# Kernel tuning notes

Hardware: AMD Instinct MI355X
Metric: run time of the kernel (lower is better)

Reference implementation:

```python
import jax, jax.numpy as jnp
import numpy as np
import math

B, S, D = 16, 4096, 64

def setup_inputs() -> dict:
    key = jax.random.key(0)
    kq, kk, kv = jax.random.split(key, 3)
    query = jax.random.normal(kq, (B, S, D), dtype=jnp.float32)
    k_ = jax.random.normal(kk, (B, S, D), dtype=jnp.float32)
    value = jax.random.normal(kv, (B, S, D), dtype=jnp.float32)
    # causal mask: 1 = allowed, 0 = masked (set to -inf), broadcast over batch
    mask = jnp.tril(jnp.ones((S, S), dtype=jnp.int32))[None, :, :]
    return {"query": query, "key": k_, "value": value, "mask": mask, "key_dim": D}

def reference(query, key, value, mask, key_dim):
    # scores: [B, S, S] = Q @ K^T / sqrt(dk)
    scores = jnp.einsum('bqd,bkd->bqk', query, key) / math.sqrt(key_dim)
    scores = jnp.where(mask == 0, -jnp.inf, scores)
    attn = jax.nn.softmax(scores, axis=-1)
    return jnp.einsum('bqk,bkd->bqd', attn, value)
```

## Files before the change

kernel.cpp:

```cpp
#include <hip/hip_runtime.h>

typedef _Float16 half8 __attribute__((ext_vector_type(8)));
typedef __fp16 fp16x2 __attribute__((ext_vector_type(2)));
typedef float f32x4 __attribute__((ext_vector_type(4)));
typedef unsigned int uint32x2 __attribute__((ext_vector_type(2)));

union Frag { half8 v; unsigned int u32[4]; uint4 u4; };
union Pack4 { _Float16 h[4]; unsigned int u[2]; };
union H2U { fp16x2 h; unsigned int u; };

constexpr int S = 4096;
constexpr int D = 64;
constexpr int NB = 16;
constexpr int LTS = 72;

__device__ __forceinline__ float ex2(float x) {
#if __has_builtin(__builtin_amdgcn_exp2f)
    return __builtin_amdgcn_exp2f(x);
#else
    return exp2f(x);
#endif
}

__global__ __launch_bounds__(256)
void prep_kernel(const float* __restrict__ K, const float* __restrict__ V,
                 _Float16* __restrict__ K16, _Float16* __restrict__ VT) {
    __shared__ float tl[64 * 66];
    const int tid = threadIdx.x;
    const int s0 = blockIdx.x * 64;
    const int b  = blockIdx.y;
    const float* Kb = K + ((size_t)b * S + s0) * D;
    const float* Vb = V + ((size_t)b * S + s0) * D;
    _Float16* K16b = K16 + ((size_t)b * S + s0) * D;

    #pragma unroll
    for (int i = 0; i < 2; ++i) {
        int e8 = tid + 256 * i;
        float4 a = ((const float4*)Kb)[2 * e8];
        float4 c = ((const float4*)Kb)[2 * e8 + 1];
        Frag f;
        f.v[0]=(_Float16)a.x; f.v[1]=(_Float16)a.y; f.v[2]=(_Float16)a.z; f.v[3]=(_Float16)a.w;
        f.v[4]=(_Float16)c.x; f.v[5]=(_Float16)c.y; f.v[6]=(_Float16)c.z; f.v[7]=(_Float16)c.w;
        ((uint4*)K16b)[e8] = f.u4;
    }
    #pragma unroll
    for (int i = 0; i < 4; ++i) {
        int fi = tid + 256 * i;
        int r = fi >> 4, c4 = (fi & 15) << 2;
        float4 v = *(const float4*)(Vb + (size_t)r * D + c4);
        float2* p = (float2*)&tl[r * 66 + c4];
        p[0] = make_float2(v.x, v.y);
        p[1] = make_float2(v.z, v.w);
    }
    __syncthreads();
    _Float16* VTb = VT + (size_t)b * D * S;
    #pragma unroll
    for (int i = 0; i < 2; ++i) {
        int fi = tid + 256 * i;
        int d = fi >> 3, s8 = (fi & 7) << 3;
        Frag f;
        #pragma unroll
        for (int j = 0; j < 8; ++j) f.v[j] = (_Float16)tl[(s8 + j) * 66 + d];
        *(uint4*)(VTb + (size_t)d * S + s0 + s8) = f.u4;
    }
}

template <int SPLIT>
__device__ __forceinline__
void fattn_body(const float* __restrict__ Q, const _Float16* __restrict__ K16,
                const _Float16* __restrict__ VT16, float* __restrict__ Out,
                _Float16* __restrict__ OP, float* __restrict__ LP,
                int b, int J, int t0, int t1, int h) {
    __shared__ __align__(16) _Float16 kt[64 * LTS];
    __shared__ __align__(16) _Float16 vt[64 * LTS];

    const int tid  = threadIdx.x;
    const int lane = tid & 63;
    const int wave = tid >> 6;
    const int ln   = lane & 15;
    const int quad = lane >> 4;

    const float* Qb = Q + (size_t)b * S * D;
    const _Float16* Kb = K16 + (size_t)b * S * D;
    const _Float16* VTb = VT16 + (size_t)b * D * S;

    const float qscale = 0.125f * 1.44269504088896340736f;
    const int qrow_base = J * 128 + wave * 32;
    const int tw = (qrow_base + 31) >> 6;

    Frag qf[2][2];
    #pragma unroll
    for (int qg = 0; qg < 2; ++qg) {
        const float* qrow = Qb + (size_t)(qrow_base + qg * 16 + ln) * D + quad * 8;
        #pragma unroll
        for (int ks = 0; ks < 2; ++ks) {
            float4 a = *(const float4*)(qrow + ks * 32);
            float4 c = *(const float4*)(qrow + ks * 32 + 4);
            Frag f;
            f.v[0]=(_Float16)(a.x*qscale); f.v[1]=(_Float16)(a.y*qscale);
            f.v[2]=(_Float16)(a.z*qscale); f.v[3]=(_Float16)(a.w*qscale);
            f.v[4]=(_Float16)(c.x*qscale); f.v[5]=(_Float16)(c.y*qscale);
            f.v[6]=(_Float16)(c.z*qscale); f.v[7]=(_Float16)(c.w*qscale);
            qf[qg][ks] = f;
        }
    }

    f32x4 o[2][4] = {};
    float l_acc[2] = {0.f, 0.f};

    const int r0_ = tid >> 3,         c8_0 = (tid & 7) << 3;
    const int r1_ = (tid + 256) >> 3, c8_1 = ((tid + 256) & 7) << 3;
    uint4 pk0, pk1, pv0, pv1;
    auto issue = [&](int tt) {
        const int kk0 = tt * 64;
        pk0 = *(const uint4*)(Kb + (size_t)(kk0 + r0_) * D + c8_0);
        pv0 = *(const uint4*)(VTb + (size_t)r0_ * S + kk0 + c8_0);
        pk1 = *(const uint4*)(Kb + (size_t)(kk0 + r1_) * D + c8_1);
        pv1 = *(const uint4*)(VTb + (size_t)r1_ * S + kk0 + c8_1);
    };
    if (t0 < t1) issue(t0);

    for (int t = t0; t < t1; ++t) {
        const int k0 = t * 64;
        __syncthreads();
        *(uint4*)(kt + r0_ * LTS + c8_0) = pk0;
        *(uint4*)(vt + r0_ * LTS + c8_0) = pv0;
        *(uint4*)(kt + r1_ * LTS + c8_1) = pk1;
        *(uint4*)(vt + r1_ * LTS + c8_1) = pv1;
        __syncthreads();
        if (t + 1 < t1) issue(t + 1);

        #pragma unroll
        for (int ks = 0; ks < 2; ++ks) {
            unsigned w[2][2][2];
            #pragma unroll
            for (int cl = 0; cl < 2; ++cl) {
                const int ct = ks * 2 + cl;
                Frag kf0, kf1;
                kf0.u4 = *(const uint4*)(kt + (ct * 16 + ln) * LTS + quad * 8);
                kf1.u4 = *(const uint4*)(kt + (ct * 16 + ln) * LTS + 32 + quad * 8);
                #pragma unroll
                for (int qg = 0; qg < 2; ++qg) {
                    f32x4 acc = {0.f, 0.f, 0.f, 0.f};
                    acc = __builtin_amdgcn_mfma_f32_16x16x32_f16(kf0.v, qf[qg][0].v, acc, 0, 0, 0);
                    acc = __builtin_amdgcn_mfma_f32_16x16x32_f16(kf1.v, qf[qg][1].v, acc, 0, 0, 0);
                    if (t >= tw) {
                        int keyb = k0 + ct * 16 + quad * 4;
                        int qrow = qrow_base + qg * 16 + ln;
                        #pragma unroll
                        for (int r = 0; r < 4; ++r)
                            if (keyb + r > qrow) acc[r] = -1e30f;
                    }
                    float p0 = ex2(acc[0]), p1 = ex2(acc[1]);
                    float p2 = ex2(acc[2]), p3 = ex2(acc[3]);
                    l_acc[qg] += (p0 + p1) + (p2 + p3);
#if __has_builtin(__builtin_amdgcn_cvt_pkrtz)
                    H2U c0, c1;
                    c0.h = __builtin_amdgcn_cvt_pkrtz(p0, p1);
                    c1.h = __builtin_amdgcn_cvt_pkrtz(p2, p3);
                    w[qg][cl][0] = c0.u;
                    w[qg][cl][1] = c1.u;
#else
                    Pack4 pk;
                    pk.h[0] = (_Float16)p0; pk.h[1] = (_Float16)p1;
                    pk.h[2] = (_Float16)p2; pk.h[3] = (_Float16)p3;
                    w[qg][cl][0] = pk.u[0];
                    w[qg][cl][1] = pk.u[1];
#endif
                }
            }

            Frag pf[2];
            #pragma unroll
            for (int qg = 0; qg < 2; ++qg) {
                unsigned x0 = w[qg][0][0], y0 = w[qg][1][0];
                unsigned x1 = w[qg][0][1], y1 = w[qg][1][1];
#if __has_builtin(__builtin_amdgcn_permlane32_swap) && __has_builtin(__builtin_amdgcn_permlane16_swap)
                uint32x2 r;
                r = __builtin_amdgcn_permlane32_swap(x0, y0, false, false); x0 = r[0]; y0 = r[1];
                r = __builtin_amdgcn_permlane32_swap(x1, y1, false, false); x1 = r[0]; y1 = r[1];
                r = __builtin_amdgcn_permlane16_swap(x0, y0, false, false); x0 = r[0]; y0 = r[1];
                r = __builtin_amdgcn_permlane16_swap(x1, y1, false, false); x1 = r[0]; y1 = r[1];
#else
                asm volatile("s_nop 1\n\tv_permlane32_swap_b32 %0, %1\n\ts_nop 1"
                             : "+v"(x0), "+v"(y0));
                asm volatile("v_permlane32_swap_b32 %0, %1\n\ts_nop 1"
                             : "+v"(x1), "+v"(y1));
                asm volatile("v_permlane16_swap_b32 %0, %1\n\ts_nop 1"
                             : "+v"(x0), "+v"(y0));
                asm volatile("v_permlane16_swap_b32 %0, %1\n\ts_nop 1"
                             : "+v"(x1), "+v"(y1));
#endif
                pf[qg].u32[0] = x0; pf[qg].u32[1] = x1;
                pf[qg].u32[2] = y0; pf[qg].u32[3] = y1;
            }

            #pragma unroll
            for (int sub = 0; sub < 4; ++sub) {
                Frag vf;
                vf.u4 = *(const uint4*)(vt + (sub * 16 + ln) * LTS + ks * 32 + quad * 8);
                #pragma unroll
                for (int qg = 0; qg < 2; ++qg)
                    o[qg][sub] = __builtin_amdgcn_mfma_f32_16x16x32_f16(pf[qg].v, vf.v, o[qg][sub], 0, 0, 0);
            }
        }
    }

    float lf[2];
    #pragma unroll
    for (int qg = 0; qg < 2; ++qg) {
        float x = l_acc[qg];
        x += __shfl_xor(x, 16, 64);
        x += __shfl_xor(x, 32, 64);
        lf[qg] = x;
    }

    if (SPLIT) {
        _Float16* OPb = OP + (size_t)(((b * 32 + J) * 4 + h)) * 8192;
        float* LPb = LP + (size_t)(((b * 32 + J) * 4 + h)) * 128;
        #pragma unroll
        for (int qg = 0; qg < 2; ++qg) {
            if (quad == 0) LPb[wave * 32 + qg * 16 + ln] = lf[qg];
            #pragma unroll
            for (int r = 0; r < 4; ++r) {
                float lrow = __shfl(lf[qg], quad * 4 + r, 64);
                float inv = (lrow > 0.f) ? (1.0f / lrow) : 0.f;
                #pragma unroll
                for (int sub = 0; sub < 4; ++sub)
                    OPb[(wave * 32 + qg * 16 + quad * 4 + r) * 64 + sub * 16 + ln] =
                        (_Float16)(o[qg][sub][r] * inv);
            }
        }
    } else {
        float* Ob = Out + (size_t)b * S * D;
        #pragma unroll
        for (int qg = 0; qg < 2; ++qg) {
            #pragma unroll
            for (int r = 0; r < 4; ++r) {
                float lrow = __shfl(lf[qg], quad * 4 + r, 64);
                float inv = 1.0f / lrow;
                #pragma unroll
                for (int sub = 0; sub < 4; ++sub)
                    Ob[(size_t)(qrow_base + qg * 16 + quad * 4 + r) * D + sub * 16 + ln] =
                        o[qg][sub][r] * inv;
            }
        }
    }
}

__global__ __launch_bounds__(256, 4)
void fattn_split_kernel(const float* __restrict__ Q, const _Float16* __restrict__ K16,
                        const _Float16* __restrict__ VT16,
                        _Float16* __restrict__ OP, float* __restrict__ LP) {
    const int bx = blockIdx.x;
    const int J = 31 - (bx >> 6);
    const int h = (bx >> 4) & 3;
    const int b = bx & 15;
    const int n  = 2 * J + 2;
    const int t0 = (h * n) >> 2;
    const int t1 = ((h + 1) * n) >> 2;
    fattn_body<1>(Q, K16, VT16, nullptr, OP, LP, b, J, t0, t1, h);
}

__global__ __launch_bounds__(256, 4)
void fattn_kernel(const float* __restrict__ Q, const _Float16* __restrict__ K16,
                  const _Float16* __restrict__ VT16, float* __restrict__ Out) {
    const int bx = blockIdx.x;
    const int J = 31 - (bx >> 4);
    const int b = bx & 15;
    fattn_body<0>(Q, K16, VT16, Out, nullptr, nullptr, b, J, 0, 2 * J + 2, 0);
}

__global__ __launch_bounds__(256)
void reduce_kernel(const _Float16* __restrict__ OP, const float* __restrict__ LP,
                   float* __restrict__ Out) {
    const int rb = blockIdx.x;
    const int b  = rb & 15;
    const int J  = rb >> 4;
    const int tid = threadIdx.x;
    const _Float16* p = OP + (size_t)(b * 32 + J) * 4 * 8192;
    const float* l = LP + (size_t)(b * 32 + J) * 4 * 128;
    float* Ob = Out + (size_t)b * S * D + (size_t)J * 8192;
    #pragma unroll
    for (int i = 0; i < 4; ++i) {
        int e8 = tid + 256 * i;
        int q  = e8 >> 3;
        float lw[4], lsum = 0.f;
        #pragma unroll
        for (int hh = 0; hh < 4; ++hh) { lw[hh] = l[hh * 128 + q]; lsum += lw[hh]; }
        float inv = 1.0f / lsum;
        float acc[8] = {};
        #pragma unroll
        for (int hh = 0; hh < 4; ++hh) {
            half8 v = *(const half8*)(p + (size_t)hh * 8192 + e8 * 8);
            #pragma unroll
            for (int j = 0; j < 8; ++j) acc[j] += lw[hh] * (float)v[j];
        }
        float4 r0, r1;
        r0.x = acc[0]*inv; r0.y = acc[1]*inv; r0.z = acc[2]*inv; r0.w = acc[3]*inv;
        r1.x = acc[4]*inv; r1.y = acc[5]*inv; r1.z = acc[6]*inv; r1.w = acc[7]*inv;
        ((float4*)Ob)[2 * e8]     = r0;
        ((float4*)Ob)[2 * e8 + 1] = r1;
    }
}

extern "C" void kernel_launch(void* const* d_in, const int* in_sizes, int n_in,
                              void* d_out, int out_size, void* d_ws, size_t ws_size,
                              hipStream_t stream) {
    const float* Q = (const float*)d_in[0];
    const float* K = (const float*)d_in[1];
    const float* V = (const float*)d_in[2];
    float* O = (float*)d_out;

    const size_t prepBytes = (size_t)NB * S * D * 2;
    _Float16* K16  = (_Float16*)d_ws;
    _Float16* VT16 = (_Float16*)((char*)d_ws + prepBytes);

    const size_t opOff = 2 * prepBytes;
    const size_t opBytes = (size_t)NB * 32 * 4 * 8192 * 2;
    const size_t lpOff = opOff + opBytes;
    const size_t lpBytes = (size_t)NB * 32 * 4 * 128 * 4;
    const size_t need = lpOff + lpBytes;

    hipLaunchKernelGGL(prep_kernel, dim3(S / 64, NB), dim3(256), 0, stream, K, V, K16, VT16);

    if (ws_size >= need) {
        _Float16* OP = (_Float16*)((char*)d_ws + opOff);
        float* LP = (float*)((char*)d_ws + lpOff);
        hipLaunchKernelGGL(fattn_split_kernel, dim3(128 * NB), dim3(256), 0, stream,
                           Q, K16, VT16, OP, LP);
        hipLaunchKernelGGL(reduce_kernel, dim3(32 * NB), dim3(256), 0, stream, OP, LP, O);
    } else {
        hipLaunchKernelGGL(fattn_kernel, dim3(32 * NB), dim3(256), 0, stream, Q, K16, VT16, O);
    }
}
```

Measured before the change: 186.6 us.

## Fuse split-K reduction into attention kernel via last-block atomic counter

Removes the separate reduce kernel launch. Each split block increments a per-(batch, query-tile) atomic counter after writing its partial output, and the fourth block to finish performs the weighted combine and writes the final output. Counters are zeroed in the prep kernel. This saves a launch and lets the reduction overlap other tiles' work, at the cost of fences, an atomic per block, and extra register and LDS pressure in the main kernel.

```diff
diff --git a/kernel.cpp b/kernel.cpp
--- a/kernel.cpp
+++ b/kernel.cpp
@@ -24,11 +24,13 @@
 
 __global__ __launch_bounds__(256)
 void prep_kernel(const float* __restrict__ K, const float* __restrict__ V,
-                 _Float16* __restrict__ K16, _Float16* __restrict__ VT) {
+                 _Float16* __restrict__ K16, _Float16* __restrict__ VT,
+                 int* __restrict__ CNT) {
     __shared__ float tl[64 * 66];
     const int tid = threadIdx.x;
     const int s0 = blockIdx.x * 64;
     const int b  = blockIdx.y;
+    if (b == 0 && blockIdx.x < 2) CNT[blockIdx.x * 256 + tid] = 0;
     const float* Kb = K + ((size_t)b * S + s0) * D;
     const float* Vb = V + ((size_t)b * S + s0) * D;
     _Float16* K16b = K16 + ((size_t)b * S + s0) * D;
@@ -70,9 +72,11 @@
 void fattn_body(const float* __restrict__ Q, const _Float16* __restrict__ K16,
                 const _Float16* __restrict__ VT16, float* __restrict__ Out,
                 _Float16* __restrict__ OP, float* __restrict__ LP,
+                int* __restrict__ CNT,
                 int b, int J, int t0, int t1, int h) {
     __shared__ __align__(16) _Float16 kt[64 * LTS];
     __shared__ __align__(16) _Float16 vt[64 * LTS];
+    __shared__ int last_flag;
 
     const int tid  = threadIdx.x;
     const int lane = tid & 63;
@@ -231,6 +235,42 @@
                         (_Float16)(o[qg][sub][r] * inv);
             }
         }
+
+        __threadfence();
+        __syncthreads();
+        if (tid == 0) {
+            int old = __hip_atomic_fetch_add(&CNT[b * 32 + J], 1,
+                                             __ATOMIC_ACQ_REL, __HIP_MEMORY_SCOPE_AGENT);
+            last_flag = (old == 3);
+        }
+        __syncthreads();
+        if (!last_flag) return;
+        __threadfence();
+
+        const _Float16* p = OP + (size_t)(b * 32 + J) * 4 * 8192;
+        const float* l = LP + (size_t)(b * 32 + J) * 4 * 128;
+        float* Ob = Out + (size_t)b * S * D + (size_t)J * 8192;
+        #pragma unroll
+        for (int i = 0; i < 4; ++i) {
+            int e8 = tid + 256 * i;
+            int q  = e8 >> 3;
+            float lw[4], lsum = 0.f;
+            #pragma unroll
+            for (int hh = 0; hh < 4; ++hh) { lw[hh] = l[hh * 128 + q]; lsum += lw[hh]; }
+            float inv = 1.0f / lsum;
+            float acc[8] = {};
+            #pragma unroll
+            for (int hh = 0; hh < 4; ++hh) {
+                half8 v = *(const half8*)(p + (size_t)hh * 8192 + e8 * 8);
+                #pragma unroll
+                for (int j = 0; j < 8; ++j) acc[j] += lw[hh] * (float)v[j];
+            }
+            float4 r0, r1;
+            r0.x = acc[0]*inv; r0.y = acc[1]*inv; r0.z = acc[2]*inv; r0.w = acc[3]*inv;
+            r1.x = acc[4]*inv; r1.y = acc[5]*inv; r1.z = acc[6]*inv; r1.w = acc[7]*inv;
+            ((float4*)Ob)[2 * e8]     = r0;
+            ((float4*)Ob)[2 * e8 + 1] = r1;
+        }
     } else {
         float* Ob = Out + (size_t)b * S * D;
         #pragma unroll
@@ -251,7 +291,8 @@
 __global__ __launch_bounds__(256, 4)
 void fattn_split_kernel(const float* __restrict__ Q, const _Float16* __restrict__ K16,
                         const _Float16* __restrict__ VT16,
-                        _Float16* __restrict__ OP, float* __restrict__ LP) {
+                        _Float16* __restrict__ OP, float* __restrict__ LP,
+                        int* __restrict__ CNT, float* __restrict__ Out) {
     const int bx = blockIdx.x;
     const int J = 31 - (bx >> 6);
     const int h = (bx >> 4) & 3;
@@ -259,7 +300,7 @@
     const int n  = 2 * J + 2;
     const int t0 = (h * n) >> 2;
     const int t1 = ((h + 1) * n) >> 2;
-    fattn_body<1>(Q, K16, VT16, nullptr, OP, LP, b, J, t0, t1, h);
+    fattn_body<1>(Q, K16, VT16, Out, OP, LP, CNT, b, J, t0, t1, h);
 }
 
 __global__ __launch_bounds__(256, 4)
@@ -268,40 +309,7 @@
     const int bx = blockIdx.x;
     const int J = 31 - (bx >> 4);
     const int b = bx & 15;
-    fattn_body<0>(Q, K16, VT16, Out, nullptr, nullptr, b, J, 0, 2 * J + 2, 0);
-}
-
-__global__ __launch_bounds__(256)
-void reduce_kernel(const _Float16* __restrict__ OP, const float* __restrict__ LP,
-                   float* __restrict__ Out) {
-    const int rb = blockIdx.x;
-    const int b  = rb & 15;
-    const int J  = rb >> 4;
-    const int tid = threadIdx.x;
-    const _Float16* p = OP + (size_t)(b * 32 + J) * 4 * 8192;
-    const float* l = LP + (size_t)(b * 32 + J) * 4 * 128;
-    float* Ob = Out + (size_t)b * S * D + (size_t)J * 8192;
-    #pragma unroll
-    for (int i = 0; i < 4; ++i) {
-        int e8 = tid + 256 * i;
-        int q  = e8 >> 3;
-        float lw[4], lsum = 0.f;
-        #pragma unroll
-        for (int hh = 0; hh < 4; ++hh) { lw[hh] = l[hh * 128 + q]; lsum += lw[hh]; }
-        float inv = 1.0f / lsum;
-        float acc[8] = {};
-        #pragma unroll
-        for (int hh = 0; hh < 4; ++hh) {
-            half8 v = *(const half8*)(p + (size_t)hh * 8192 + e8 * 8);
-            #pragma unroll
-            for (int j = 0; j < 8; ++j) acc[j] += lw[hh] * (float)v[j];
-        }
-        float4 r0, r1;
-        r0.x = acc[0]*inv; r0.y = acc[1]*inv; r0.z = acc[2]*inv; r0.w = acc[3]*inv;
-        r1.x = acc[4]*inv; r1.y = acc[5]*inv; r1.z = acc[6]*inv; r1.w = acc[7]*inv;
-        ((float4*)Ob)[2 * e8]     = r0;
-        ((float4*)Ob)[2 * e8 + 1] = r1;
-    }
+    fattn_body<0>(Q, K16, VT16, Out, nullptr, nullptr, nullptr, b, J, 0, 2 * J + 2, 0);
 }
 
 extern "C" void kernel_launch(void* const* d_in, const int* in_sizes, int n_in,
@@ -320,16 +328,18 @@
     const size_t opBytes = (size_t)NB * 32 * 4 * 8192 * 2;
     const size_t lpOff = opOff + opBytes;
     const size_t lpBytes = (size_t)NB * 32 * 4 * 128 * 4;
-    const size_t need = lpOff + lpBytes;
-
-    hipLaunchKernelGGL(prep_kernel, dim3(S / 64, NB), dim3(256), 0, stream, K, V, K16, VT16);
+    const size_t cntOff = lpOff + lpBytes;
+    const size_t cntBytes = 512 * sizeof(int);
+    const size_t need = cntOff + cntBytes;
+
+    int* CNT = (int*)((char*)d_ws + cntOff);
+    hipLaunchKernelGGL(prep_kernel, dim3(S / 64, NB), dim3(256), 0, stream, K, V, K16, VT16, CNT);
 
     if (ws_size >= need) {
         _Float16* OP = (_Float16*)((char*)d_ws + opOff);
         float* LP = (float*)((char*)d_ws + lpOff);
         hipLaunchKernelGGL(fattn_split_kernel, dim3(128 * NB), dim3(256), 0, stream,
-                           Q, K16, VT16, OP, LP);
-        hipLaunchKernelGGL(reduce_kernel, dim3(32 * NB), dim3(256), 0, stream, OP, LP, O);
+                           Q, K16, VT16, OP, LP, CNT, O);
     } else {
         hipLaunchKernelGGL(fattn_kernel, dim3(32 * NB), dim3(256), 0, stream, Q, K16, VT16, O);
     }
```

Result: slower. 611.6 us (+227.8%).

## Fuse K/V fp16 conversion and V transpose into attention kernel, drop prep pass

Applied to the files above, without the earlier changes.

Removes the separate prep kernel that converted K to fp16 and wrote a transposed fp16 V to workspace. The attention kernel now loads fp32 K and V tiles directly, converts them in registers, and transposes V through an extra shared-memory staging buffer, with V prefetched two tiles ahead. This saves one kernel launch and the workspace write and read-back, but doubles the global bytes loaded per tile (fp32 instead of fp16) across the many redundant causal tile reads. It also adds conversion work, more LDS traffic and an extra shared buffer that may hurt occupancy.

```diff
diff --git a/kernel.cpp b/kernel.cpp
--- a/kernel.cpp
+++ b/kernel.cpp
@@ -6,7 +6,6 @@
 typedef unsigned int uint32x2 __attribute__((ext_vector_type(2)));
 
 union Frag { half8 v; unsigned int u32[4]; uint4 u4; };
-union Pack4 { _Float16 h[4]; unsigned int u[2]; };
 union H2U { fp16x2 h; unsigned int u; };
 
 constexpr int S = 4096;
@@ -22,57 +21,38 @@
 #endif
 }
 
-__global__ __launch_bounds__(256)
-void prep_kernel(const float* __restrict__ K, const float* __restrict__ V,
-                 _Float16* __restrict__ K16, _Float16* __restrict__ VT) {
-    __shared__ float tl[64 * 66];
-    const int tid = threadIdx.x;
-    const int s0 = blockIdx.x * 64;
-    const int b  = blockIdx.y;
-    const float* Kb = K + ((size_t)b * S + s0) * D;
-    const float* Vb = V + ((size_t)b * S + s0) * D;
-    _Float16* K16b = K16 + ((size_t)b * S + s0) * D;
-
-    #pragma unroll
-    for (int i = 0; i < 2; ++i) {
-        int e8 = tid + 256 * i;
-        float4 a = ((const float4*)Kb)[2 * e8];
-        float4 c = ((const float4*)Kb)[2 * e8 + 1];
-        Frag f;
-        f.v[0]=(_Float16)a.x; f.v[1]=(_Float16)a.y; f.v[2]=(_Float16)a.z; f.v[3]=(_Float16)a.w;
-        f.v[4]=(_Float16)c.x; f.v[5]=(_Float16)c.y; f.v[6]=(_Float16)c.z; f.v[7]=(_Float16)c.w;
-        ((uint4*)K16b)[e8] = f.u4;
-    }
-    #pragma unroll
-    for (int i = 0; i < 4; ++i) {
-        int fi = tid + 256 * i;
-        int r = fi >> 4, c4 = (fi & 15) << 2;
-        float4 v = *(const float4*)(Vb + (size_t)r * D + c4);
-        float2* p = (float2*)&tl[r * 66 + c4];
-        p[0] = make_float2(v.x, v.y);
-        p[1] = make_float2(v.z, v.w);
-    }
-    __syncthreads();
-    _Float16* VTb = VT + (size_t)b * D * S;
-    #pragma unroll
-    for (int i = 0; i < 2; ++i) {
-        int fi = tid + 256 * i;
-        int d = fi >> 3, s8 = (fi & 7) << 3;
-        Frag f;
-        #pragma unroll
-        for (int j = 0; j < 8; ++j) f.v[j] = (_Float16)tl[(s8 + j) * 66 + d];
-        *(uint4*)(VTb + (size_t)d * S + s0 + s8) = f.u4;
-    }
+__device__ __forceinline__ void cvt16(const float4* a, uint4& lo, uint4& hi) {
+#if __has_builtin(__builtin_amdgcn_cvt_pkrtz)
+    H2U h0,h1,h2,h3,h4,h5,h6,h7;
+    h0.h = __builtin_amdgcn_cvt_pkrtz(a[0].x, a[0].y);
+    h1.h = __builtin_amdgcn_cvt_pkrtz(a[0].z, a[0].w);
+    h2.h = __builtin_amdgcn_cvt_pkrtz(a[1].x, a[1].y);
+    h3.h = __builtin_amdgcn_cvt_pkrtz(a[1].z, a[1].w);
+    h4.h = __builtin_amdgcn_cvt_pkrtz(a[2].x, a[2].y);
+    h5.h = __builtin_amdgcn_cvt_pkrtz(a[2].z, a[2].w);
+    h6.h = __builtin_amdgcn_cvt_pkrtz(a[3].x, a[3].y);
+    h7.h = __builtin_amdgcn_cvt_pkrtz(a[3].z, a[3].w);
+    lo = make_uint4(h0.u, h1.u, h2.u, h3.u);
+    hi = make_uint4(h4.u, h5.u, h6.u, h7.u);
+#else
+    Frag f, g;
+    f.v[0]=(_Float16)a[0].x; f.v[1]=(_Float16)a[0].y; f.v[2]=(_Float16)a[0].z; f.v[3]=(_Float16)a[0].w;
+    f.v[4]=(_Float16)a[1].x; f.v[5]=(_Float16)a[1].y; f.v[6]=(_Float16)a[1].z; f.v[7]=(_Float16)a[1].w;
+    g.v[0]=(_Float16)a[2].x; g.v[1]=(_Float16)a[2].y; g.v[2]=(_Float16)a[2].z; g.v[3]=(_Float16)a[2].w;
+    g.v[4]=(_Float16)a[3].x; g.v[5]=(_Float16)a[3].y; g.v[6]=(_Float16)a[3].z; g.v[7]=(_Float16)a[3].w;
+    lo = f.u4; hi = g.u4;
+#endif
 }
 
 template <int SPLIT>
 __device__ __forceinline__
-void fattn_body(const float* __restrict__ Q, const _Float16* __restrict__ K16,
-                const _Float16* __restrict__ VT16, float* __restrict__ Out,
+void fattn_body(const float* __restrict__ Q, const float* __restrict__ K,
+                const float* __restrict__ V, float* __restrict__ Out,
                 _Float16* __restrict__ OP, float* __restrict__ LP,
                 int b, int J, int t0, int t1, int h) {
     __shared__ __align__(16) _Float16 kt[64 * LTS];
     __shared__ __align__(16) _Float16 vt[64 * LTS];
+    __shared__ __align__(16) _Float16 vs[64 * LTS];
 
     const int tid  = threadIdx.x;
     const int lane = tid & 63;
@@ -81,8 +61,8 @@
     const int quad = lane >> 4;
 
     const float* Qb = Q + (size_t)b * S * D;
-    const _Float16* Kb = K16 + (size_t)b * S * D;
-    const _Float16* VTb = VT16 + (size_t)b * D * S;
+    const float* Kb = K + (size_t)b * S * D;
+    const float* Vb = V + (size_t)b * S * D;
 
     const float qscale = 0.125f * 1.44269504088896340736f;
     const int qrow_base = J * 128 + wave * 32;
@@ -108,27 +88,59 @@
     f32x4 o[2][4] = {};
     float l_acc[2] = {0.f, 0.f};
 
-    const int r0_ = tid >> 3,         c8_0 = (tid & 7) << 3;
-    const int r1_ = (tid + 256) >> 3, c8_1 = ((tid + 256) & 7) << 3;
-    uint4 pk0, pk1, pv0, pv1;
-    auto issue = [&](int tt) {
-        const int kk0 = tt * 64;
-        pk0 = *(const uint4*)(Kb + (size_t)(kk0 + r0_) * D + c8_0);
-        pv0 = *(const uint4*)(VTb + (size_t)r0_ * S + kk0 + c8_0);
-        pk1 = *(const uint4*)(Kb + (size_t)(kk0 + r1_) * D + c8_1);
-        pv1 = *(const uint4*)(VTb + (size_t)r1_ * S + kk0 + c8_1);
+    const int sr = tid >> 2;
+    const int sq = (tid & 3) << 4;
+    const int td2 = tid >> 3;
+    const int ts8 = (tid & 7) << 3;
+
+    float4 kA[4], vA[4];
+    auto loadK = [&](int tt) {
+        const float4* p = (const float4*)(Kb + (size_t)(tt * 64 + sr) * D + sq);
+        kA[0] = p[0]; kA[1] = p[1]; kA[2] = p[2]; kA[3] = p[3];
     };
-    if (t0 < t1) issue(t0);
+    auto loadV = [&](int tt) {
+        const float4* p = (const float4*)(Vb + (size_t)(tt * 64 + sr) * D + sq);
+        vA[0] = p[0]; vA[1] = p[1]; vA[2] = p[2]; vA[3] = p[3];
+    };
+
+    if (t0 < t1) {
+        loadV(t0); loadK(t0);
+        uint4 lo, hi; cvt16(vA, lo, hi);
+        *(uint4*)(vs + sr * LTS + sq)     = lo;
+        *(uint4*)(vs + sr * LTS + sq + 8) = hi;
+        loadV(t0 + 1 < t1 ? t0 + 1 : t0);
+    }
 
     for (int t = t0; t < t1; ++t) {
         const int k0 = t * 64;
         __syncthreads();
-        *(uint4*)(kt + r0_ * LTS + c8_0) = pk0;
-        *(uint4*)(vt + r0_ * LTS + c8_0) = pv0;
-        *(uint4*)(kt + r1_ * LTS + c8_1) = pk1;
-        *(uint4*)(vt + r1_ * LTS + c8_1) = pv1;
+
+        {
+            uint4 lo, hi; cvt16(kA, lo, hi);
+            *(uint4*)(kt + sr * LTS + sq)     = lo;
+            *(uint4*)(kt + sr * LTS + sq + 8) = hi;
+        }
+        {
+            const unsigned* col = (const unsigned*)vs + ts8 * (LTS / 2) + td2;
+            unsigned x0 = col[0],   x1 = col[36],  x2 = col[72],  x3 = col[108];
+            unsigned x4 = col[144], x5 = col[180], x6 = col[216], x7 = col[252];
+            uint4 rlo, rhi;
+            rlo.x = (x0 & 0xffffu) | (x1 << 16);  rlo.y = (x2 & 0xffffu) | (x3 << 16);
+            rlo.z = (x4 & 0xffffu) | (x5 << 16);  rlo.w = (x6 & 0xffffu) | (x7 << 16);
+            rhi.x = (x0 >> 16) | (x1 & 0xffff0000u);  rhi.y = (x2 >> 16) | (x3 & 0xffff0000u);
+            rhi.z = (x4 >> 16) | (x5 & 0xffff0000u);  rhi.w = (x6 >> 16) | (x7 & 0xffff0000u);
+            *(uint4*)(vt + (2 * td2) * LTS + ts8)     = rlo;
+            *(uint4*)(vt + (2 * td2 + 1) * LTS + ts8) = rhi;
+        }
         __syncthreads();
-        if (t + 1 < t1) issue(t + 1);
+
+        if (t + 1 < t1) {
+            uint4 lo, hi; cvt16(vA, lo, hi);
+            *(uint4*)(vs + sr * LTS + sq)     = lo;
+            *(uint4*)(vs + sr * LTS + sq + 8) = hi;
+            loadK(t + 1);
+            loadV(t + 2 < t1 ? t + 2 : t + 1);
+        }
 
         #pragma unroll
         for (int ks = 0; ks < 2; ++ks) {
@@ -161,11 +173,11 @@
                     w[qg][cl][0] = c0.u;
                     w[qg][cl][1] = c1.u;
 #else
-                    Pack4 pk;
-                    pk.h[0] = (_Float16)p0; pk.h[1] = (_Float16)p1;
-                    pk.h[2] = (_Float16)p2; pk.h[3] = (_Float16)p3;
-                    w[qg][cl][0] = pk.u[0];
-                    w[qg][cl][1] = pk.u[1];
+                    Frag pk;
+                    pk.v[0] = (_Float16)p0; pk.v[1] = (_Float16)p1;
+                    pk.v[2] = (_Float16)p2; pk.v[3] = (_Float16)p3;
+                    w[qg][cl][0] = pk.u32[0];
+                    w[qg][cl][1] = pk.u32[1];
 #endif
                 }
             }
@@ -249,8 +261,8 @@
 }
 
 __global__ __launch_bounds__(256, 4)
-void fattn_split_kernel(const float* __restrict__ Q, const _Float16* __restrict__ K16,
-                        const _Float16* __restrict__ VT16,
+void fattn_split_kernel(const float* __restrict__ Q, const float* __restrict__ K,
+                        const float* __restrict__ V,
                         _Float16* __restrict__ OP, float* __restrict__ LP) {
     const int bx = blockIdx.x;
     const int J = 31 - (bx >> 6);
@@ -259,16 +271,16 @@
     const int n  = 2 * J + 2;
     const int t0 = (h * n) >> 2;
     const int t1 = ((h + 1) * n) >> 2;
-    fattn_body<1>(Q, K16, VT16, nullptr, OP, LP, b, J, t0, t1, h);
+    fattn_body<1>(Q, K, V, nullptr, OP, LP, b, J, t0, t1, h);
 }
 
 __global__ __launch_bounds__(256, 4)
-void fattn_kernel(const float* __restrict__ Q, const _Float16* __restrict__ K16,
-                  const _Float16* __restrict__ VT16, float* __restrict__ Out) {
+void fattn_kernel(const float* __restrict__ Q, const float* __restrict__ K,
+                  const float* __restrict__ V, float* __restrict__ Out) {
     const int bx = blockIdx.x;
     const int J = 31 - (bx >> 4);
     const int b = bx & 15;
-    fattn_body<0>(Q, K16, VT16, Out, nullptr, nullptr, b, J, 0, 2 * J + 2, 0);
+    fattn_body<0>(Q, K, V, Out, nullptr, nullptr, b, J, 0, 2 * J + 2, 0);
 }
 
 __global__ __launch_bounds__(256)
@@ -312,25 +324,17 @@
     const float* V = (const float*)d_in[2];
     float* O = (float*)d_out;
 
-    const size_t prepBytes = (size_t)NB * S * D * 2;
-    _Float16* K16  = (_Float16*)d_ws;
-    _Float16* VT16 = (_Float16*)((char*)d_ws + prepBytes);
-
-    const size_t opOff = 2 * prepBytes;
     const size_t opBytes = (size_t)NB * 32 * 4 * 8192 * 2;
-    const size_t lpOff = opOff + opBytes;
     const size_t lpBytes = (size_t)NB * 32 * 4 * 128 * 4;
-    const size_t need = lpOff + lpBytes;
-
-    hipLaunchKernelGGL(prep_kernel, dim3(S / 64, NB), dim3(256), 0, stream, K, V, K16, VT16);
+    const size_t need = opBytes + lpBytes;
 
     if (ws_size >= need) {
-        _Float16* OP = (_Float16*)((char*)d_ws + opOff);
-        float* LP = (float*)((char*)d_ws + lpOff);
+        _Float16* OP = (_Float16*)d_ws;
+        float* LP = (float*)((char*)d_ws + opBytes);
         hipLaunchKernelGGL(fattn_split_kernel, dim3(128 * NB), dim3(256), 0, stream,
-                           Q, K16, VT16, OP, LP);
+                           Q, K, V, OP, LP);
         hipLaunchKernelGGL(reduce_kernel, dim3(32 * NB), dim3(256), 0, stream, OP, LP, O);
     } else {
-        hipLaunchKernelGGL(fattn_kernel, dim3(32 * NB), dim3(256), 0, stream, Q, K16, VT16, O);
-    }
-}
+        hipLaunchKernelGGL(fattn_kernel, dim3(32 * NB), dim3(256), 0, stream, Q, K, V, O);
+    }
+}
```

New measurement: 268.9 us. 44.1% more time.

## Split causal KV range into variable chunk counts per query block

Applied to the files above, without the earlier changes.

Replaces the fixed four-way KV split per query block with a split whose chunk count grows with the causal length of the block (1 to 7 chunks, 125 slots per batch). Every split block then processes a similar number of KV tiles, which balances the causal workload and drops near-empty blocks for early rows. The cost is a small index search loop at block start, a variable-length loop in the reduce kernel, and a grid of 2000 blocks instead of 2048.

```diff
diff --git a/kernel.cpp b/kernel.cpp
--- a/kernel.cpp
+++ b/kernel.cpp
@@ -13,6 +13,11 @@
 constexpr int D = 64;
 constexpr int NB = 16;
 constexpr int LTS = 72;
+constexpr int NCH = 125;
+
+__device__ __forceinline__ int chunks_of(int J) {
+    return J < 4 ? 1 : J < 9 ? 2 : J < 14 ? 3 : J < 19 ? 4 : J < 24 ? 5 : J < 29 ? 6 : 7;
+}
 
 __device__ __forceinline__ float ex2(float x) {
 #if __has_builtin(__builtin_amdgcn_exp2f)
@@ -70,7 +75,7 @@
 void fattn_body(const float* __restrict__ Q, const _Float16* __restrict__ K16,
                 const _Float16* __restrict__ VT16, float* __restrict__ Out,
                 _Float16* __restrict__ OP, float* __restrict__ LP,
-                int b, int J, int t0, int t1, int h) {
+                int b, int J, int t0, int t1, int slot) {
     __shared__ __align__(16) _Float16 kt[64 * LTS];
     __shared__ __align__(16) _Float16 vt[64 * LTS];
 
@@ -216,8 +221,8 @@
     }
 
     if (SPLIT) {
-        _Float16* OPb = OP + (size_t)(((b * 32 + J) * 4 + h)) * 8192;
-        float* LPb = LP + (size_t)(((b * 32 + J) * 4 + h)) * 128;
+        _Float16* OPb = OP + ((size_t)b * NCH + slot) * 8192;
+        float* LPb = LP + ((size_t)b * NCH + slot) * 128;
         #pragma unroll
         for (int qg = 0; qg < 2; ++qg) {
             if (quad == 0) LPb[wave * 32 + qg * 16 + ln] = lf[qg];
@@ -253,13 +258,20 @@
                         const _Float16* __restrict__ VT16,
                         _Float16* __restrict__ OP, float* __restrict__ LP) {
     const int bx = blockIdx.x;
-    const int J = 31 - (bx >> 6);
-    const int h = (bx >> 4) & 3;
     const int b = bx & 15;
+    const int g = bx >> 4;
+    int off = 0, J = 0;
+    for (;;) {
+        int c = chunks_of(J);
+        if (g < off + c) break;
+        off += c; ++J;
+    }
+    const int c  = chunks_of(J);
+    const int ci = g - off;
     const int n  = 2 * J + 2;
-    const int t0 = (h * n) >> 2;
-    const int t1 = ((h + 1) * n) >> 2;
-    fattn_body<1>(Q, K16, VT16, nullptr, OP, LP, b, J, t0, t1, h);
+    const int t0 = (ci * n) / c;
+    const int t1 = ((ci + 1) * n) / c;
+    fattn_body<1>(Q, K16, VT16, nullptr, OP, LP, b, J, t0, t1, g);
 }
 
 __global__ __launch_bounds__(256, 4)
@@ -278,23 +290,25 @@
     const int b  = rb & 15;
     const int J  = rb >> 4;
     const int tid = threadIdx.x;
-    const _Float16* p = OP + (size_t)(b * 32 + J) * 4 * 8192;
-    const float* l = LP + (size_t)(b * 32 + J) * 4 * 128;
+    int off = 0;
+    for (int jj = 0; jj < J; ++jj) off += chunks_of(jj);
+    const int c = chunks_of(J);
+    const _Float16* p = OP + ((size_t)b * NCH + off) * 8192;
+    const float* l = LP + ((size_t)b * NCH + off) * 128;
     float* Ob = Out + (size_t)b * S * D + (size_t)J * 8192;
     #pragma unroll
     for (int i = 0; i < 4; ++i) {
         int e8 = tid + 256 * i;
         int q  = e8 >> 3;
-        float lw[4], lsum = 0.f;
-        #pragma unroll
-        for (int hh = 0; hh < 4; ++hh) { lw[hh] = l[hh * 128 + q]; lsum += lw[hh]; }
+        float lsum = 0.f;
+        for (int hh = 0; hh < c; ++hh) lsum += l[hh * 128 + q];
         float inv = 1.0f / lsum;
         float acc[8] = {};
-        #pragma unroll
-        for (int hh = 0; hh < 4; ++hh) {
+        for (int hh = 0; hh < c; ++hh) {
+            float w = l[hh * 128 + q];
             half8 v = *(const half8*)(p + (size_t)hh * 8192 + e8 * 8);
             #pragma unroll
-            for (int j = 0; j < 8; ++j) acc[j] += lw[hh] * (float)v[j];
+            for (int j = 0; j < 8; ++j) acc[j] += w * (float)v[j];
         }
         float4 r0, r1;
         r0.x = acc[0]*inv; r0.y = acc[1]*inv; r0.z = acc[2]*inv; r0.w = acc[3]*inv;
@@ -317,9 +331,9 @@
     _Float16* VT16 = (_Float16*)((char*)d_ws + prepBytes);
 
     const size_t opOff = 2 * prepBytes;
-    const size_t opBytes = (size_t)NB * 32 * 4 * 8192 * 2;
+    const size_t opBytes = (size_t)NB * NCH * 8192 * 2;
     const size_t lpOff = opOff + opBytes;
-    const size_t lpBytes = (size_t)NB * 32 * 4 * 128 * 4;
+    const size_t lpBytes = (size_t)NB * NCH * 128 * 4;
     const size_t need = lpOff + lpBytes;
 
     hipLaunchKernelGGL(prep_kernel, dim3(S / 64, NB), dim3(256), 0, stream, K, V, K16, VT16);
@@ -327,7 +341,7 @@
     if (ws_size >= need) {
         _Float16* OP = (_Float16*)((char*)d_ws + opOff);
         float* LP = (float*)((char*)d_ws + lpOff);
-        hipLaunchKernelGGL(fattn_split_kernel, dim3(128 * NB), dim3(256), 0, stream,
+        hipLaunchKernelGGL(fattn_split_kernel, dim3(NCH * NB), dim3(256), 0, stream,
                            Q, K16, VT16, OP, LP);
         hipLaunchKernelGGL(reduce_kernel, dim3(32 * NB), dim3(256), 0, stream, OP, LP, O);
     } else {
```

Result: slower. 200.0 us (+7.2%).
